# Kernel optimization log

Hardware: AMD Instinct MI355X
Metric: run time of the kernel (lower is better)

## Reference

```python
import jax, jax.numpy as jnp
import numpy as np

B, T, ND, DH, DZ = 32, 4096, 32, 128, 128
IN_DIM = 2 * ND + DH  # 192


def setup_inputs() -> dict:
    key = jax.random.key(0)
    ks = jax.random.split(key, 11)
    s = 1.0 / np.sqrt(DZ)  # PyTorch GRUCell init scale
    return {
        "z0": jax.random.normal(ks[0], (B, DZ), jnp.float32),
        # sorted irregular timestamps per series
        "t_dyn": jnp.sort(jax.random.uniform(ks[1], (B, T), jnp.float32) * 100.0, axis=1),
        "Y_dyn": jax.random.normal(ks[2], (B, T, ND), jnp.float32),
        "M_dyn": (jax.random.uniform(ks[3], (B, T, ND)) > 0.5).astype(jnp.float32),
        "dyn_lens": jax.random.randint(ks[4], (B,), 1, T + 1, dtype=jnp.int32),
        "h_path_vals": jax.random.normal(ks[5], (B, T, DH), jnp.float32),
        "W_ih": jax.random.uniform(ks[6], (3 * DZ, IN_DIM), jnp.float32, -s, s),
        "b_ih": jax.random.uniform(ks[7], (3 * DZ,), jnp.float32, -s, s),
        "W_hh": jax.random.uniform(ks[8], (3 * DZ, DZ), jnp.float32, -s, s),
        "b_hh": jax.random.uniform(ks[9], (3 * DZ,), jnp.float32, -s, s),
        "log_gamma": jnp.zeros((DZ,), jnp.float32),
    }


def reference(z0, t_dyn, Y_dyn, M_dyn, dyn_lens, h_path_vals, W_ih, b_ih, W_hh, b_hh, log_gamma):
    gamma = jax.nn.softplus(log_gamma)  # (d_z,)
    Tm = t_dyn.shape[1]
    # concat dynamic features once; precompute all input-side gate projections as one big GEMM
    x = jnp.concatenate([Y_dyn, M_dyn, h_path_vals], axis=-1)        # (B,T,IN_DIM)
    gi_all = jnp.einsum('bti,gi->btg', x, W_ih) + b_ih               # (B,T,3*d_z)
    active = (jnp.arange(Tm)[:, None] < dyn_lens[None, :]).astype(z0.dtype)  # (T,B)

    def step(carry, xs):
        z, t_prev = carry
        t_k, gi, a = xs                 # (B,), (B,3dz), (B,)
        dt = jnp.maximum(t_k - t_prev, 0.0)
        z_d = z * jnp.exp(-gamma * dt[:, None])      # exponential decay
        gh = z_d @ W_hh.T + b_hh
        i_r, i_u, i_n = jnp.split(gi, 3, axis=-1)
        h_r, h_u, h_n = jnp.split(gh, 3, axis=-1)
        r = jax.nn.sigmoid(i_r + h_r)
        u = jax.nn.sigmoid(i_u + h_u)
        n = jnp.tanh(i_n + r * h_n)
        z_new = (1.0 - u) * n + u * z_d
        am = a[:, None]
        z_out = am * z_new + (1.0 - am) * z_d        # length masking
        return (z_out, t_k), z_out

    xs = (t_dyn.T, jnp.swapaxes(gi_all, 0, 1), active)  # time-major
    (z_final, _), Z = jax.lax.scan(step, (z0, t_dyn[:, 0]), xs)
    Z_traj = jnp.swapaxes(Z, 0, 1)                      # (B,T,d_z)
    return z_final, Z_traj
```

## Files before the change

kernel.cpp:

```cpp
#include <hip/hip_runtime.h>
#include <hip/hip_bf16.h>
#include <stdint.h>

typedef unsigned short u16;

#define NB  32
#define NT  4096
#define NDZ 128
#define NG  384
#define NIN 192

__device__ __forceinline__ float rlane(float v, int k) {
  return __int_as_float(__builtin_amdgcn_readlane(__float_as_int(v), k));
}
__device__ __forceinline__ float fast_rcp(float x) { return __builtin_amdgcn_rcpf(x); }
__device__ __forceinline__ float sigmoid_f(float x) { return fast_rcp(1.f + __expf(-x)); }
__device__ __forceinline__ float tanh_f(float x) {
  return 1.f - 2.f * fast_rcp(1.f + __expf(2.f * x));
}
__device__ __forceinline__ u16 f2bf(float f) {
  unsigned u = __float_as_uint(f);
  return (u16)((u + 0x7fffu + ((u >> 16) & 1u)) >> 16);
}
__device__ __forceinline__ float bf2f(u16 u) { return __uint_as_float((unsigned)u << 16); }

__device__ __forceinline__ void bar_lds() {
  asm volatile("s_waitcnt lgkmcnt(0)\n\ts_barrier" ::: "memory");
}

__device__ __forceinline__ float giload(const float* p) { return *p; }
__device__ __forceinline__ float giload(const u16* p)   { return bf2f(*p); }
__device__ __forceinline__ void store8(float* p, const float* v) {
  float4 a = {v[0], v[1], v[2], v[3]}, b = {v[4], v[5], v[6], v[7]};
  *(float4*)p = a; *(float4*)(p + 4) = b;
}
__device__ __forceinline__ void store8(u16* p, const float* v) {
  uint4 o;
  o.x = (unsigned)f2bf(v[0]) | ((unsigned)f2bf(v[1]) << 16);
  o.y = (unsigned)f2bf(v[2]) | ((unsigned)f2bf(v[3]) << 16);
  o.z = (unsigned)f2bf(v[4]) | ((unsigned)f2bf(v[5]) << 16);
  o.w = (unsigned)f2bf(v[6]) | ((unsigned)f2bf(v[7]) << 16);
  *(uint4*)p = o;
}

#define GM 128
#define GN 128
#define LDSS 132

template <typename GT>
__global__ __launch_bounds__(256) void gemm_gi(
    const float* __restrict__ Y, const float* __restrict__ M,
    const float* __restrict__ H, const float* __restrict__ Wih,
    const float* __restrict__ bih, GT* __restrict__ gi)
{
  __shared__ float As[32 * LDSS];
  __shared__ float Bs[32 * LDSS];
  const int tid = threadIdx.x;
  const size_t m0 = (size_t)blockIdx.x * GM;
  const int n0 = blockIdx.y * GN;
  const int tm = tid & 15;
  const int tn = tid >> 4;

  float acc[8][8];
#pragma unroll
  for (int i = 0; i < 8; ++i)
#pragma unroll
    for (int j = 0; j < 8; ++j) acc[i][j] = 0.f;

#pragma unroll
  for (int kc = 0; kc < 6; ++kc) {
    const float* src; int stride; int off;
    if (kc == 0)      { src = Y; stride = 32;  off = 0; }
    else if (kc == 1) { src = M; stride = 32;  off = 0; }
    else              { src = H; stride = 128; off = (kc - 2) * 32; }
#pragma unroll
    for (int it = 0; it < 4; ++it) {
      int x = tid + it * 256;
      int row = x >> 3, q = x & 7;
      float4 v = *(const float4*)(src + (m0 + (size_t)row) * stride + off + q * 4);
      As[(q * 4 + 0) * LDSS + row] = v.x;
      As[(q * 4 + 1) * LDSS + row] = v.y;
      As[(q * 4 + 2) * LDSS + row] = v.z;
      As[(q * 4 + 3) * LDSS + row] = v.w;
    }
#pragma unroll
    for (int it = 0; it < 4; ++it) {
      int x = tid + it * 256;
      int g = x >> 3, q = x & 7;
      float4 v = *(const float4*)(Wih + (size_t)(n0 + g) * NIN + kc * 32 + q * 4);
      Bs[(q * 4 + 0) * LDSS + g] = v.x;
      Bs[(q * 4 + 1) * LDSS + g] = v.y;
      Bs[(q * 4 + 2) * LDSS + g] = v.z;
      Bs[(q * 4 + 3) * LDSS + g] = v.w;
    }
    __syncthreads();
#pragma unroll
    for (int kk = 0; kk < 32; ++kk) {
      float4 a0 = *(const float4*)&As[kk * LDSS + tm * 8];
      float4 a1 = *(const float4*)&As[kk * LDSS + tm * 8 + 4];
      float4 b0 = *(const float4*)&Bs[kk * LDSS + tn * 8];
      float4 b1 = *(const float4*)&Bs[kk * LDSS + tn * 8 + 4];
      float av[8] = {a0.x, a0.y, a0.z, a0.w, a1.x, a1.y, a1.z, a1.w};
      float bv[8] = {b0.x, b0.y, b0.z, b0.w, b1.x, b1.y, b1.z, b1.w};
#pragma unroll
      for (int i = 0; i < 8; ++i)
#pragma unroll
        for (int j = 0; j < 8; ++j)
          acc[i][j] = __builtin_fmaf(av[i], bv[j], acc[i][j]);
    }
    __syncthreads();
  }
  float bv[8];
#pragma unroll
  for (int j = 0; j < 8; ++j) bv[j] = bih[n0 + tn * 8 + j];
#pragma unroll
  for (int i = 0; i < 8; ++i) {
    size_t row = m0 + (size_t)(tm * 8 + i);
    GT* o = gi + row * NG + n0 + tn * 8;
    float v[8];
#pragma unroll
    for (int j = 0; j < 8; ++j) v[j] = acc[i][j] + bv[j];
    store8(o, v);
  }
}

#define KS 32

template <typename GT>
__global__ __launch_bounds__(256, 1) void scan_k(
    const float* __restrict__ zinit, const float* __restrict__ tdyn,
    const int* __restrict__ lens, const float* __restrict__ Whh,
    const float* __restrict__ bhh, const float* __restrict__ lgam,
    const GT* __restrict__ gi, float* __restrict__ out)
{
  const int b = blockIdx.x;
  const int tid = threadIdx.x;
  const int lane = tid & 63;
  const int w = tid >> 6;
  const int k0 = w * KS;
  const int e = lane & 31;
  const int hi = lane >> 5;
  const int j = k0 + e;

  __shared__ float P0[4][NG];
  __shared__ float P1[4][NG];

  float2 wp[3][KS];
#pragma unroll
  for (int p = 0; p < 3; ++p) {
    const float4* r0 = (const float4*)(Whh + (size_t)(lane + 128 * p) * NDZ + k0);
    const float4* r1 = (const float4*)(Whh + (size_t)(lane + 128 * p + 64) * NDZ + k0);
#pragma unroll
    for (int q = 0; q < 8; ++q) {
      float4 v0 = r0[q];
      float4 v1 = r1[q];
      wp[p][4 * q + 0].x = v0.x; wp[p][4 * q + 0].y = v1.x;
      wp[p][4 * q + 1].x = v0.y; wp[p][4 * q + 1].y = v1.y;
      wp[p][4 * q + 2].x = v0.z; wp[p][4 * q + 2].y = v1.z;
      wp[p][4 * q + 3].x = v0.w; wp[p][4 * q + 3].y = v1.w;
    }
  }

  const int len = lens[b];
  const float* tp = tdyn + (size_t)b * NT;
  const GT* gb = gi + (size_t)b * NT * NG;
  float* traj = out + (size_t)NB * NDZ + (size_t)b * NT * NDZ;

  float zc = zinit[b * NDZ + j];
  const float lg = lgam[j];
  const float gam = (lg > 15.f) ? lg : __logf(1.f + __expf(lg));
  const float br = bhh[j], bu = bhh[NDZ + j], bn = bhh[2 * NDZ + j];
  float t_prev = tp[0];
  float zdr = zc;

  const int prow = hi ? (NDZ + j) : j;
  const int nrow = 2 * NDZ + j;
  const int nq = hi * 2;

  float ptkA = tp[1];
  float ptkB = tp[2];
  float pgrA = giload(gb + j), pguA = giload(gb + NDZ + j), pgnA = giload(gb + 2 * NDZ + j);
  float pgrB = giload(gb + NG + j), pguB = giload(gb + NG + NDZ + j), pgnB = giload(gb + NG + 2 * NDZ + j);

  auto stepf = [&](float (*PB)[NG], float& ptkX, float& pgrX, float& pguX, float& pgnX, int t) {
    const bool active = (t < len);
    if (active) {
      float2 a0 = {0.f, 0.f}, a1 = {0.f, 0.f}, a2 = {0.f, 0.f};
#pragma unroll
      for (int k = 0; k < KS; ++k) {
        const float zk = rlane(zdr, k);
        a0.x = __builtin_fmaf(wp[0][k].x, zk, a0.x);
        a0.y = __builtin_fmaf(wp[0][k].y, zk, a0.y);
        a1.x = __builtin_fmaf(wp[1][k].x, zk, a1.x);
        a1.y = __builtin_fmaf(wp[1][k].y, zk, a1.y);
        a2.x = __builtin_fmaf(wp[2][k].x, zk, a2.x);
        a2.y = __builtin_fmaf(wp[2][k].y, zk, a2.y);
      }
      PB[w][lane]       = a0.x;  PB[w][lane + 64]  = a0.y;
      PB[w][lane + 128] = a1.x;  PB[w][lane + 192] = a1.y;
      PB[w][lane + 256] = a2.x;  PB[w][lane + 320] = a2.y;
    }
    bar_lds();

    const float zd = zdr;
    if (active) {
      const float p0 = PB[0][prow], p1 = PB[1][prow];
      const float p2 = PB[2][prow], p3 = PB[3][prow];
      const float n0 = PB[nq][nrow], n1 = PB[nq + 1][nrow];
      const float prim = (p0 + p1) + (p2 + p3);
      const float n2 = n0 + n1;
      const float oth = __shfl(prim, lane ^ 32, 64);
      const float nx  = __shfl(n2,   lane ^ 32, 64);
      const float snv = n2 + nx;
      const float sr = hi ? oth  : prim;
      const float su = hi ? prim : oth;
      const float r = sigmoid_f(sr + br + pgrX);
      const float u = sigmoid_f(su + bu + pguX);
      const float n = tanh_f(__builtin_fmaf(r, snv + bn, pgnX));
      zc = (1.f - u) * n + u * zd;
    } else {
      zc = zd;
    }
    if (lane < 32) traj[(size_t)t * NDZ + j] = zc;

    const float tk = ptkX;
    const float dt = fmaxf(tk - t_prev, 0.f);
    zdr = zc * __expf(-gam * dt);
    t_prev = tk;

    const int t2 = (t + 2 < NT) ? (t + 2) : (NT - 1);
    const int t3 = (t + 3 < NT) ? (t + 3) : (NT - 1);
    ptkX = tp[t3];
    const GT* g2 = gb + (size_t)t2 * NG;
    pgrX = giload(g2 + j);
    pguX = giload(g2 + NDZ + j);
    pgnX = giload(g2 + 2 * NDZ + j);
  };

  for (int t = 0; t < NT; t += 2) {
    stepf(P0, ptkA, pgrA, pguA, pgnA, t);
    stepf(P1, ptkB, pgrB, pguB, pgnB, t + 1);
  }
  if (lane < 32) out[b * NDZ + j] = zc;
}

extern "C" void kernel_launch(void* const* d_in, const int* in_sizes, int n_in,
                              void* d_out, int out_size, void* d_ws, size_t ws_size,
                              hipStream_t stream) {
  const float* z0   = (const float*)d_in[0];
  const float* tdyn = (const float*)d_in[1];
  const float* Y    = (const float*)d_in[2];
  const float* M    = (const float*)d_in[3];
  const int*   lens = (const int*)d_in[4];
  const float* H    = (const float*)d_in[5];
  const float* Wih  = (const float*)d_in[6];
  const float* bih  = (const float*)d_in[7];
  const float* Whh  = (const float*)d_in[8];
  const float* bhh  = (const float*)d_in[9];
  const float* lgam = (const float*)d_in[10];
  float* out = (float*)d_out;

  const size_t needF32 = (size_t)NB * NT * NG * sizeof(float);
  dim3 ggrid((NB * NT) / GM, NG / GN);
  if (ws_size >= needF32) {
    float* gi = (float*)d_ws;
    gemm_gi<float><<<ggrid, 256, 0, stream>>>(Y, M, H, Wih, bih, gi);
    scan_k<float><<<dim3(NB), 256, 0, stream>>>(z0, tdyn, lens, Whh, bhh, lgam, gi, out);
  } else {
    u16* gi = (u16*)d_ws;
    gemm_gi<u16><<<ggrid, 256, 0, stream>>>(Y, M, H, Wih, bih, gi);
    scan_k<u16><<<dim3(NB), 256, 0, stream>>>(z0, tdyn, lens, Whh, bhh, lgam, gi, out);
  }
}
```

Before: 3.541 ms.

## Split scan gate rows across two wave groups using 512-thread blocks

The recurrent scan kernel now runs 8 waves per batch block instead of 4. The waves form two halves, and each half computes a disjoint set of gate rows of the hidden-to-hidden matvec, so each lane does 3 FMA chains per k instead of 6. Both halves redundantly compute the gate nonlinearities and the new state, and only one half writes the trajectory. The decay exponential is also computed at the start of each step so it sits off the post-barrier critical path. In exchange, 8 waves now join every barrier, and the 96 weight registers per lane under launch_bounds(512,2) may push register pressure close to spilling.

```diff
diff --git a/kernel.cpp b/kernel.cpp
--- a/kernel.cpp
+++ b/kernel.cpp
@@ -127,7 +127,7 @@
 #define KS 32
 
 template <typename GT>
-__global__ __launch_bounds__(256, 1) void scan_k(
+__global__ __launch_bounds__(512, 2) void scan_k(
     const float* __restrict__ zinit, const float* __restrict__ tdyn,
     const int* __restrict__ lens, const float* __restrict__ Whh,
     const float* __restrict__ bhh, const float* __restrict__ lgam,
@@ -137,7 +137,9 @@
   const int tid = threadIdx.x;
   const int lane = tid & 63;
   const int w = tid >> 6;
-  const int k0 = w * KS;
+  const int s_idx = w & 3;
+  const int h = w >> 2;
+  const int k0 = s_idx * KS;
   const int e = lane & 31;
   const int hi = lane >> 5;
   const int j = k0 + e;
@@ -145,19 +147,20 @@
   __shared__ float P0[4][NG];
   __shared__ float P1[4][NG];
 
-  float2 wp[3][KS];
-#pragma unroll
-  for (int p = 0; p < 3; ++p) {
-    const float4* r0 = (const float4*)(Whh + (size_t)(lane + 128 * p) * NDZ + k0);
-    const float4* r1 = (const float4*)(Whh + (size_t)(lane + 128 * p + 64) * NDZ + k0);
+  const int rowA = h * NDZ + lane;
+  const int rowB = rowA + 64;
+  const int rowC = 2 * NDZ + h * 64 + lane;
+  float wa[KS], wb[KS], wc[KS];
+  {
+    const float4* ra = (const float4*)(Whh + (size_t)rowA * NDZ + k0);
+    const float4* rb = (const float4*)(Whh + (size_t)rowB * NDZ + k0);
+    const float4* rc = (const float4*)(Whh + (size_t)rowC * NDZ + k0);
 #pragma unroll
     for (int q = 0; q < 8; ++q) {
-      float4 v0 = r0[q];
-      float4 v1 = r1[q];
-      wp[p][4 * q + 0].x = v0.x; wp[p][4 * q + 0].y = v1.x;
-      wp[p][4 * q + 1].x = v0.y; wp[p][4 * q + 1].y = v1.y;
-      wp[p][4 * q + 2].x = v0.z; wp[p][4 * q + 2].y = v1.z;
-      wp[p][4 * q + 3].x = v0.w; wp[p][4 * q + 3].y = v1.w;
+      float4 va = ra[q], vb = rb[q], vc = rc[q];
+      wa[4 * q + 0] = va.x; wa[4 * q + 1] = va.y; wa[4 * q + 2] = va.z; wa[4 * q + 3] = va.w;
+      wb[4 * q + 0] = vb.x; wb[4 * q + 1] = vb.y; wb[4 * q + 2] = vb.z; wb[4 * q + 3] = vb.w;
+      wc[4 * q + 0] = vc.x; wc[4 * q + 1] = vc.y; wc[4 * q + 2] = vc.z; wc[4 * q + 3] = vc.w;
     }
   }
 
@@ -183,22 +186,23 @@
   float pgrB = giload(gb + NG + j), pguB = giload(gb + NG + NDZ + j), pgnB = giload(gb + NG + 2 * NDZ + j);
 
   auto stepf = [&](float (*PB)[NG], float& ptkX, float& pgrX, float& pguX, float& pgnX, int t) {
+    const float tk = ptkX;
+    const float ef = __expf(-gam * fmaxf(tk - t_prev, 0.f));
+    t_prev = tk;
+
     const bool active = (t < len);
     if (active) {
-      float2 a0 = {0.f, 0.f}, a1 = {0.f, 0.f}, a2 = {0.f, 0.f};
+      float aa = 0.f, ab = 0.f, ac = 0.f;
 #pragma unroll
       for (int k = 0; k < KS; ++k) {
         const float zk = rlane(zdr, k);
-        a0.x = __builtin_fmaf(wp[0][k].x, zk, a0.x);
-        a0.y = __builtin_fmaf(wp[0][k].y, zk, a0.y);
-        a1.x = __builtin_fmaf(wp[1][k].x, zk, a1.x);
-        a1.y = __builtin_fmaf(wp[1][k].y, zk, a1.y);
-        a2.x = __builtin_fmaf(wp[2][k].x, zk, a2.x);
-        a2.y = __builtin_fmaf(wp[2][k].y, zk, a2.y);
+        aa = __builtin_fmaf(wa[k], zk, aa);
+        ab = __builtin_fmaf(wb[k], zk, ab);
+        ac = __builtin_fmaf(wc[k], zk, ac);
       }
-      PB[w][lane]       = a0.x;  PB[w][lane + 64]  = a0.y;
-      PB[w][lane + 128] = a1.x;  PB[w][lane + 192] = a1.y;
-      PB[w][lane + 256] = a2.x;  PB[w][lane + 320] = a2.y;
+      PB[s_idx][rowA] = aa;
+      PB[s_idx][rowB] = ab;
+      PB[s_idx][rowC] = ac;
     }
     bar_lds();
 
@@ -214,19 +218,17 @@
       const float snv = n2 + nx;
       const float sr = hi ? oth  : prim;
       const float su = hi ? prim : oth;
-      const float r = sigmoid_f(sr + br + pgrX);
-      const float u = sigmoid_f(su + bu + pguX);
-      const float n = tanh_f(__builtin_fmaf(r, snv + bn, pgnX));
+      const float cr = br + pgrX, cu = bu + pguX, cn = bn;
+      const float r = sigmoid_f(sr + cr);
+      const float u = sigmoid_f(su + cu);
+      const float n = tanh_f(__builtin_fmaf(r, snv + cn, pgnX));
       zc = (1.f - u) * n + u * zd;
     } else {
       zc = zd;
     }
-    if (lane < 32) traj[(size_t)t * NDZ + j] = zc;
-
-    const float tk = ptkX;
-    const float dt = fmaxf(tk - t_prev, 0.f);
-    zdr = zc * __expf(-gam * dt);
-    t_prev = tk;
+    if (h == 0 && lane < 32) traj[(size_t)t * NDZ + j] = zc;
+
+    zdr = zc * ef;
 
     const int t2 = (t + 2 < NT) ? (t + 2) : (NT - 1);
     const int t3 = (t + 3 < NT) ? (t + 3) : (NT - 1);
@@ -241,7 +243,7 @@
     stepf(P0, ptkA, pgrA, pguA, pgnA, t);
     stepf(P1, ptkB, pgrB, pguB, pgnB, t + 1);
   }
-  if (lane < 32) out[b * NDZ + j] = zc;
+  if (h == 0 && lane < 32) out[b * NDZ + j] = zc;
 }
 
 extern "C" void kernel_launch(void* const* d_in, const int* in_sizes, int n_in,
@@ -265,10 +267,10 @@
   if (ws_size >= needF32) {
     float* gi = (float*)d_ws;
     gemm_gi<float><<<ggrid, 256, 0, stream>>>(Y, M, H, Wih, bih, gi);
-    scan_k<float><<<dim3(NB), 256, 0, stream>>>(z0, tdyn, lens, Whh, bhh, lgam, gi, out);
+    scan_k<float><<<dim3(NB), 512, 0, stream>>>(z0, tdyn, lens, Whh, bhh, lgam, gi, out);
   } else {
     u16* gi = (u16*)d_ws;
     gemm_gi<u16><<<ggrid, 256, 0, stream>>>(Y, M, H, Wih, bih, gi);
-    scan_k<u16><<<dim3(NB), 256, 0, stream>>>(z0, tdyn, lens, Whh, bhh, lgam, gi, out);
-  }
-}
+    scan_k<u16><<<dim3(NB), 512, 0, stream>>>(z0, tdyn, lens, Whh, bhh, lgam, gi, out);
+  }
+}
```

Result: no change. 3.548 ms (+0.2%).
